# Kernel optimization log

Measured on AMD Instinct MI355X. Metric: run time of the kernel, lower is better.

The kernel has to match this reference:

```python
import jax, jax.numpy as jnp
import numpy as np

HEAD = 12
HEAD_DIM = 64  # dim // head = 768 // 12


def setup_inputs() -> dict:
    key = jax.random.key(0)
    k1, k2, k3 = jax.random.split(key, 3)
    B, N, D = 4, 2048, 768
    scale = 1.0 / np.sqrt(D)
    return {
        "x": jax.random.normal(k1, (B, N, D), dtype=jnp.float32),
        "w_qkv": jax.random.normal(k2, (D, 3 * D), dtype=jnp.float32) * scale,
        "w_proj": jax.random.normal(k3, (D, D), dtype=jnp.float32) * scale,
        "b_proj": jnp.zeros((D,), dtype=jnp.float32),
    }


def reference(x, w_qkv, w_proj, b_proj):
    B, N, D = x.shape
    qkv = x @ w_qkv  # [B, N, 3D]
    q, k, v = jnp.split(qkv, 3, axis=-1)
    # [B, H, N, k]
    def heads(t):
        return t.reshape(B, N, HEAD, HEAD_DIM).transpose(0, 2, 1, 3)
    q, k, v = heads(q), heads(k), heads(v)
    attn = jnp.einsum("bhnd,bhmd->bhnm", q, k) / jnp.sqrt(jnp.float32(HEAD_DIM))
    attn_prob = jax.nn.softmax(attn, axis=-1)  # dropout p=0.0 -> identity
    out = jnp.einsum("bhnm,bhmd->bhnd", attn_prob, v)
    out = out.transpose(0, 2, 1, 3).reshape(B, N, D)
    return out @ w_proj + b_proj
```

## Files before the change

### kernel.cpp

```cpp
#include <hip/hip_runtime.h>

typedef unsigned short u16;
typedef unsigned int u32;
typedef u16 u16x4 __attribute__((ext_vector_type(4)));
typedef u16 u16x8 __attribute__((ext_vector_type(8)));
typedef u32 u32x4 __attribute__((ext_vector_type(4)));
typedef __bf16 bf16x8 __attribute__((ext_vector_type(8)));
typedef float f32x4 __attribute__((ext_vector_type(4)));
typedef float f32x16 __attribute__((ext_vector_type(16)));

#define MFMA16 __builtin_amdgcn_mfma_f32_16x16x32_bf16
#define MFMA32 __builtin_amdgcn_mfma_f32_32x32x16_bf16

__device__ __forceinline__ u16 f2bf(float f) {
  return __builtin_bit_cast(u16, (__bf16)f);
}

__device__ __forceinline__ u32 pk2bf(float a, float b) {
  return (u32)__builtin_bit_cast(u16, (__bf16)a) |
         ((u32)__builtin_bit_cast(u16, (__bf16)b) << 16);
}

__device__ __forceinline__ void gload_lds16(const void* g, void* l) {
  __builtin_amdgcn_global_load_lds(
      (const __attribute__((address_space(1))) u32*)g,
      (__attribute__((address_space(3))) u32*)l, 16, 0, 0);
}

__global__ void cvt_f32_bf16_kernel(const float* __restrict__ in,
                                    u16* __restrict__ out, int n4) {
  int i = blockIdx.x * blockDim.x + threadIdx.x;
  if (i >= n4) return;
  float4 v = reinterpret_cast<const float4*>(in)[i];
  u16x4 o;
  o[0] = f2bf(v.x); o[1] = f2bf(v.y); o[2] = f2bf(v.z); o[3] = f2bf(v.w);
  reinterpret_cast<u16x4*>(out)[i] = o;
}

__global__ void transpose_cvt_kernel(const float* __restrict__ w,
                                     u16* __restrict__ wt, int K, int N) {
  __shared__ float t[32][33];
  int bk = blockIdx.x * 32, bn = blockIdx.y * 32;
  int x = threadIdx.x, y = threadIdx.y;
#pragma unroll
  for (int j = 0; j < 32; j += 8)
    t[y + j][x] = w[(size_t)(bk + y + j) * N + bn + x];
  __syncthreads();
#pragma unroll
  for (int j = 0; j < 32; j += 8)
    wt[(size_t)(bn + y + j) * K + bk + x] = f2bf(t[x][y + j]);
}

#define QSCALE 0.18033688011112042f

template <int NTOT, int EPI>
__global__ __launch_bounds__(256)
void gemm_bf16_kernel(const u16* __restrict__ A, const u16* __restrict__ BT,
                      u16* __restrict__ qo, u16* __restrict__ ko,
                      u16* __restrict__ vt, float* __restrict__ outF,
                      const float* __restrict__ bias) {
  __shared__ u16 sh[16384];
  u16* As = sh;
  u16* Bs = sh + 8192;
  const int tid = threadIdx.x;
  const int l = tid & 63, w = tid >> 6;
  const int lr = l & 15, lg = l >> 4;
  const int mtile = blockIdx.x & 63;
  const int ntile = blockIdx.x >> 6;
  const int mbase = mtile * 128, nbase = ntile * 128;
  const int wr = (w >> 1) * 64, wc = (w & 1) * 64;

  f32x4 acc[4][4] = {};

  for (int k0 = 0; k0 < 768; k0 += 64) {
#pragma unroll
    for (int i = 0; i < 4; ++i) {
      const int c = w * 64 + i * 256 + l;
      const int row = c >> 3, c16 = c & 7;
      const int sc = c16 ^ (row & 7);
      gload_lds16(A + (size_t)(mbase + row) * 768 + k0 + sc * 8,
                  &As[(size_t)(w * 64 + i * 256) * 8]);
      gload_lds16(BT + (size_t)(nbase + row) * 768 + k0 + sc * 8,
                  &Bs[(size_t)(w * 64 + i * 256) * 8]);
    }
    __syncthreads();
#pragma unroll
    for (int ks = 0; ks < 2; ++ks) {
      bf16x8 af[4], bfr[4];
#pragma unroll
      for (int m = 0; m < 4; ++m) {
        const int row = wr + m * 16 + lr;
        const int byte = (row * 128 + ks * 64 + lg * 16) ^ ((row & 7) << 4);
        af[m] = *reinterpret_cast<const bf16x8*>((const char*)As + byte);
      }
#pragma unroll
      for (int n = 0; n < 4; ++n) {
        const int row = wc + n * 16 + lr;
        const int byte = (row * 128 + ks * 64 + lg * 16) ^ ((row & 7) << 4);
        bfr[n] = *reinterpret_cast<const bf16x8*>((const char*)Bs + byte);
      }
#pragma unroll
      for (int m = 0; m < 4; ++m)
#pragma unroll
        for (int n = 0; n < 4; ++n)
          acc[m][n] = MFMA16(af[m], bfr[n], acc[m][n], 0, 0, 0);
    }
    __syncthreads();
  }

  if (EPI == 0 && ntile >= 12) {
    u16* vts = sh;
#pragma unroll
    for (int m = 0; m < 4; ++m)
#pragma unroll
      for (int n = 0; n < 4; ++n)
#pragma unroll
        for (int r = 0; r < 4; ++r) {
          const int col = wc + n * 16 + lr;
          const int row = wr + m * 16 + lg * 4 + r;
          const int byte = col * 256 + ((row * 2) ^ ((col & 7) << 4));
          *reinterpret_cast<u16*>((char*)vts + byte) = f2bf(acc[m][n][r]);
        }
    __syncthreads();
    const int b2 = mbase >> 11, nn0 = mbase & 2047;
#pragma unroll
    for (int i = 0; i < 8; ++i) {
      const int idx = i * 256 + tid;
      const int col = idx >> 4, u = idx & 15;
      u16x8 vv = *reinterpret_cast<u16x8*>(
          (char*)vts + (col * 256 + ((u * 16) ^ ((col & 7) << 4))));
      const int cg = nbase - 1536 + col;
      const int hh = cg >> 6, dd = cg & 63;
      *reinterpret_cast<u16x8*>(
          vt + (((size_t)(b2 * 12 + hh)) * 64 + dd) * 2048 + nn0 + u * 8) = vv;
    }
    return;
  }

#pragma unroll
  for (int m = 0; m < 4; ++m) {
#pragma unroll
    for (int n = 0; n < 4; ++n) {
#pragma unroll
      for (int r = 0; r < 4; ++r) {
        const int row = mbase + wr + m * 16 + lg * 4 + r;
        const int col = nbase + wc + n * 16 + lr;
        float val = acc[m][n][r];
        if (EPI == 0) {
          const int w2 = col / 768;
          const int c2 = col - w2 * 768;
          const int hh = c2 >> 6, dd = c2 & 63;
          const int b2 = row >> 11, nn = row & 2047;
          u16* dst = (w2 == 0) ? qo : ko;
          if (w2 == 0) val *= QSCALE;
          dst[(((size_t)(b2 * 12 + hh)) * 2048 + nn) * 64 + dd] = f2bf(val);
        } else {
          outF[(size_t)row * NTOT + col] = val + bias[col];
        }
      }
    }
  }
}

__global__ __launch_bounds__(256)
void flash_attn32_kernel(const u16* __restrict__ qb, const u16* __restrict__ kb,
                         const u16* __restrict__ vtb, u16* __restrict__ ao) {
  __shared__ u16 sh[16384];
  const int tid = threadIdx.x, w = tid >> 6, l = tid & 63;
  const int q5 = l & 31, hi = l >> 5;
  const int swz = (blockIdx.x & 7) * 96 + (blockIdx.x >> 3);
  const int bh = swz >> 4, qt = swz & 15;
  const int b = bh / 12, h = bh % 12;
  const int qrow0 = qt * 128 + w * 32;
  const u16* Q = qb + ((size_t)bh * 2048 + qrow0) * 64;
  const u16* K = kb + (size_t)bh * 2048 * 64;
  const u16* Vg = vtb + (size_t)bh * 64 * 2048;

  bf16x8 qf[4];
#pragma unroll
  for (int dk = 0; dk < 4; ++dk)
    qf[dk] = *reinterpret_cast<const bf16x8*>(Q + (size_t)q5 * 64 + dk * 16 + hi * 8);

  u16x8 ob1;
#pragma unroll
  for (int i = 0; i < 8; ++i) ob1[i] = 0x3F80;
  const bf16x8 ones = __builtin_bit_cast(bf16x8, ob1);

  f32x16 ot0 = {}, ot1 = {};
  f32x16 osum = {};

  auto stage = [&](u16* base, int kt) {
#pragma unroll
    for (int i = 0; i < 2; ++i) {
      const int c = w * 64 + i * 256 + l;
      const int row = c >> 3, sc = (c & 7) ^ (row & 7);
      gload_lds16(K + (size_t)(kt + row) * 64 + sc * 8,
                  base + (size_t)(w * 64 + i * 256) * 8);
    }
#pragma unroll
    for (int i = 0; i < 2; ++i) {
      const int c = w * 64 + i * 256 + l;
      const int row = c >> 3, sc = (c & 7) ^ (row & 7);
      gload_lds16(Vg + (size_t)row * 2048 + kt + sc * 8,
                  base + 4096 + (size_t)(w * 64 + i * 256) * 8);
    }
  };

  stage(sh, 0);
  int cur = 0;
  const int swq = (q5 & 7) << 4;

  for (int kt = 0; kt < 2048; kt += 64) {
    __syncthreads();
    u16* tb = sh + cur * 8192;
    if (kt + 64 < 2048) stage(sh + (cur ^ 1) * 8192, kt + 64);
    const char* ksb = (const char*)tb;
    const char* vsb = (const char*)(tb + 4096);

    f32x16 st0 = {}, st1 = {};
    __builtin_amdgcn_s_setprio(1);
#pragma unroll
    for (int dk = 0; dk < 4; ++dk) {
      const int off = dk * 32 + hi * 16;
      bf16x8 kf0 = *reinterpret_cast<const bf16x8*>(ksb + ((q5 * 128 + off) ^ swq));
      bf16x8 kf1 = *reinterpret_cast<const bf16x8*>(ksb + (((q5 + 32) * 128 + off) ^ swq));
      st0 = MFMA32(kf0, qf[dk], st0, 0, 0, 0);
      st1 = MFMA32(kf1, qf[dk], st1, 0, 0, 0);
    }
    __builtin_amdgcn_s_setprio(0);

#pragma unroll
    for (int r = 0; r < 16; ++r) st0[r] = __builtin_amdgcn_exp2f(st0[r]);
#pragma unroll
    for (int r = 0; r < 16; ++r) st1[r] = __builtin_amdgcn_exp2f(st1[r]);

    __builtin_amdgcn_s_setprio(1);
#pragma unroll
    for (int kvs = 0; kvs < 4; ++kvs) {
      const f32x16& stx = (kvs < 2) ? st0 : st1;
      const int rb = (kvs & 1) * 8;
      const u32 A0 = pk2bf(stx[rb + 0], stx[rb + 1]);
      const u32 A1 = pk2bf(stx[rb + 2], stx[rb + 3]);
      const u32 A2 = pk2bf(stx[rb + 4], stx[rb + 5]);
      const u32 A3 = pk2bf(stx[rb + 6], stx[rb + 7]);
      const u32 s1 = hi ? A0 : A2, s2 = hi ? A1 : A3;
      const u32 r1 = (u32)__shfl_xor((int)s1, 32);
      const u32 r2 = (u32)__shfl_xor((int)s2, 32);
      u32x4 wv;
      wv[0] = hi ? r1 : A0; wv[1] = hi ? r2 : A1;
      wv[2] = hi ? A2 : r1; wv[3] = hi ? A3 : r2;
      const bf16x8 pf = __builtin_bit_cast(bf16x8, wv);
      const int off = kvs * 32 + hi * 16;
      bf16x8 vf0 = *reinterpret_cast<const bf16x8*>(vsb + ((q5 * 128 + off) ^ swq));
      bf16x8 vf1 = *reinterpret_cast<const bf16x8*>(vsb + (((q5 + 32) * 128 + off) ^ swq));
      ot0 = MFMA32(vf0, pf, ot0, 0, 0, 0);
      ot1 = MFMA32(vf1, pf, ot1, 0, 0, 0);
      osum = MFMA32(ones, pf, osum, 0, 0, 0);
    }
    __builtin_amdgcn_s_setprio(0);
    cur ^= 1;
  }

  u16* ob = sh + w * 2048;
  const float inv = 1.0f / osum[0];
#pragma unroll
  for (int g = 0; g < 4; ++g) {
    u16x4 pk0, pk1;
#pragma unroll
    for (int r = 0; r < 4; ++r) {
      pk0[r] = f2bf(ot0[g * 4 + r] * inv);
      pk1[r] = f2bf(ot1[g * 4 + r] * inv);
    }
    const int d0 = hi * 4 + g * 8;
    *reinterpret_cast<u16x4*>((char*)ob + ((q5 * 128 + d0 * 2) ^ swq)) = pk0;
    *reinterpret_cast<u16x4*>((char*)ob + ((q5 * 128 + (d0 + 32) * 2) ^ swq)) = pk1;
  }
  __syncthreads();
#pragma unroll
  for (int i = 0; i < 4; ++i) {
    const int idx = i * 64 + l;
    const int qr = idx >> 3, cc = idx & 7;
    u16x8 vv = *reinterpret_cast<u16x8*>(
        (char*)ob + ((qr * 128 + cc * 16) ^ ((qr & 7) << 4)));
    *reinterpret_cast<u16x8*>(
        ao + ((size_t)(b * 2048 + qrow0 + qr)) * 768 + h * 64 + cc * 8) = vv;
  }
}

extern "C" void kernel_launch(void* const* d_in, const int* in_sizes, int n_in,
                              void* d_out, int out_size, void* d_ws,
                              size_t ws_size, hipStream_t stream) {
  const float* x = (const float*)d_in[0];
  const float* w_qkv = (const float*)d_in[1];
  const float* w_proj = (const float*)d_in[2];
  const float* b_proj = (const float*)d_in[3];
  float* out = (float*)d_out;

  char* ws = (char*)d_ws;
  size_t off = 0;
  auto alloc = [&](size_t bytes) {
    char* p = ws + off;
    off += (bytes + 255) & ~(size_t)255;
    return p;
  };
  u16* xb = (u16*)alloc(8192ull * 768 * 2);
  u16* wqkvT = (u16*)alloc(2304ull * 768 * 2);
  u16* wprojT = (u16*)alloc(768ull * 768 * 2);
  u16* qbuf = (u16*)alloc(48ull * 2048 * 64 * 2);
  u16* kbuf = (u16*)alloc(48ull * 2048 * 64 * 2);
  u16* vtb = (u16*)alloc(48ull * 64 * 2048 * 2);
  u16* aob = (u16*)alloc(8192ull * 768 * 2);
  (void)ws_size; (void)n_in; (void)in_sizes; (void)out_size;

  cvt_f32_bf16_kernel<<<(8192 * 768 / 4) / 256, 256, 0, stream>>>(
      x, xb, 8192 * 768 / 4);
  transpose_cvt_kernel<<<dim3(768 / 32, 2304 / 32), dim3(32, 8), 0, stream>>>(
      w_qkv, wqkvT, 768, 2304);
  transpose_cvt_kernel<<<dim3(768 / 32, 768 / 32), dim3(32, 8), 0, stream>>>(
      w_proj, wprojT, 768, 768);

  gemm_bf16_kernel<2304, 0><<<64 * 18, 256, 0, stream>>>(
      xb, wqkvT, qbuf, kbuf, vtb, nullptr, nullptr);

  flash_attn32_kernel<<<768, 256, 0, stream>>>(qbuf, kbuf, vtb, aob);

  gemm_bf16_kernel<768, 1><<<64 * 6, 256, 0, stream>>>(
      aob, wprojT, nullptr, nullptr, nullptr, out, b_proj);
}
```

Before: 178.5 us.

## Split attention KV range across wave pairs and reduce partial outputs in LDS

```diff
diff --git a/kernel.cpp b/kernel.cpp
--- a/kernel.cpp
+++ b/kernel.cpp
@@ -19,6 +19,11 @@
 __device__ __forceinline__ u32 pk2bf(float a, float b) {
   return (u32)__builtin_bit_cast(u16, (__bf16)a) |
          ((u32)__builtin_bit_cast(u16, (__bf16)b) << 16);
+}
+
+__device__ __forceinline__ float bfsum2(u32 w) {
+  return __builtin_bit_cast(float, w << 16) +
+         __builtin_bit_cast(float, w & 0xFFFF0000u);
 }
 
 __device__ __forceinline__ void gload_lds16(const void* g, void* l) {
@@ -168,10 +173,12 @@
   __shared__ u16 sh[16384];
   const int tid = threadIdx.x, w = tid >> 6, l = tid & 63;
   const int q5 = l & 31, hi = l >> 5;
-  const int swz = (blockIdx.x & 7) * 96 + (blockIdx.x >> 3);
-  const int bh = swz >> 4, qt = swz & 15;
+  const int qw = w & 1, half = w >> 1;
+  const int swz = (blockIdx.x & 7) * 192 + (blockIdx.x >> 3);
+  const int bh = swz >> 5, qt = swz & 31;
   const int b = bh / 12, h = bh % 12;
-  const int qrow0 = qt * 128 + w * 32;
+  const int qrow0 = qt * 64 + qw * 32;
+  const int kvStart = half << 10;
   const u16* Q = qb + ((size_t)bh * 2048 + qrow0) * 64;
   const u16* K = kb + (size_t)bh * 2048 * 64;
   const u16* Vg = vtb + (size_t)bh * 64 * 2048;
@@ -181,41 +188,33 @@
   for (int dk = 0; dk < 4; ++dk)
     qf[dk] = *reinterpret_cast<const bf16x8*>(Q + (size_t)q5 * 64 + dk * 16 + hi * 8);
 
-  u16x8 ob1;
-#pragma unroll
-  for (int i = 0; i < 8; ++i) ob1[i] = 0x3F80;
-  const bf16x8 ones = __builtin_bit_cast(bf16x8, ob1);
-
   f32x16 ot0 = {}, ot1 = {};
-  f32x16 osum = {};
-
-  auto stage = [&](u16* base, int kt) {
-#pragma unroll
-    for (int i = 0; i < 2; ++i) {
-      const int c = w * 64 + i * 256 + l;
+  float l_ = 0.f;
+
+  u16* Ks = sh + half * 8192;
+  u16* Vs = Ks + 4096;
+  const int swq = (q5 & 7) << 4;
+
+  for (int t = 0; t < 16; ++t) {
+    const int kt = kvStart + t * 64;
+#pragma unroll
+    for (int i = 0; i < 4; ++i) {
+      const int c = qw * 64 + i * 128 + l;
       const int row = c >> 3, sc = (c & 7) ^ (row & 7);
       gload_lds16(K + (size_t)(kt + row) * 64 + sc * 8,
-                  base + (size_t)(w * 64 + i * 256) * 8);
-    }
-#pragma unroll
-    for (int i = 0; i < 2; ++i) {
-      const int c = w * 64 + i * 256 + l;
+                  Ks + (size_t)(qw * 64 + i * 128) * 8);
+    }
+#pragma unroll
+    for (int i = 0; i < 4; ++i) {
+      const int c = qw * 64 + i * 128 + l;
       const int row = c >> 3, sc = (c & 7) ^ (row & 7);
       gload_lds16(Vg + (size_t)row * 2048 + kt + sc * 8,
-                  base + 4096 + (size_t)(w * 64 + i * 256) * 8);
-    }
-  };
-
-  stage(sh, 0);
-  int cur = 0;
-  const int swq = (q5 & 7) << 4;
-
-  for (int kt = 0; kt < 2048; kt += 64) {
-    __syncthreads();
-    u16* tb = sh + cur * 8192;
-    if (kt + 64 < 2048) stage(sh + (cur ^ 1) * 8192, kt + 64);
-    const char* ksb = (const char*)tb;
-    const char* vsb = (const char*)(tb + 4096);
+                  Vs + (size_t)(qw * 64 + i * 128) * 8);
+    }
+    __syncthreads();
+
+    const char* ksb = (const char*)Ks;
+    const char* vsb = (const char*)Vs;
 
     f32x16 st0 = {}, st1 = {};
     __builtin_amdgcn_s_setprio(1);
@@ -234,6 +233,7 @@
 #pragma unroll
     for (int r = 0; r < 16; ++r) st1[r] = __builtin_amdgcn_exp2f(st1[r]);
 
+    float ls = 0.f;
     __builtin_amdgcn_s_setprio(1);
 #pragma unroll
     for (int kvs = 0; kvs < 4; ++kvs) {
@@ -243,6 +243,7 @@
       const u32 A1 = pk2bf(stx[rb + 2], stx[rb + 3]);
       const u32 A2 = pk2bf(stx[rb + 4], stx[rb + 5]);
       const u32 A3 = pk2bf(stx[rb + 6], stx[rb + 7]);
+      ls += (bfsum2(A0) + bfsum2(A1)) + (bfsum2(A2) + bfsum2(A3));
       const u32 s1 = hi ? A0 : A2, s2 = hi ? A1 : A3;
       const u32 r1 = (u32)__shfl_xor((int)s1, 32);
       const u32 r2 = (u32)__shfl_xor((int)s2, 32);
@@ -255,35 +256,58 @@
       bf16x8 vf1 = *reinterpret_cast<const bf16x8*>(vsb + (((q5 + 32) * 128 + off) ^ swq));
       ot0 = MFMA32(vf0, pf, ot0, 0, 0, 0);
       ot1 = MFMA32(vf1, pf, ot1, 0, 0, 0);
-      osum = MFMA32(ones, pf, osum, 0, 0, 0);
     }
     __builtin_amdgcn_s_setprio(0);
-    cur ^= 1;
-  }
-
-  u16* ob = sh + w * 2048;
-  const float inv = 1.0f / osum[0];
-#pragma unroll
-  for (int g = 0; g < 4; ++g) {
-    u16x4 pk0, pk1;
-#pragma unroll
-    for (int r = 0; r < 4; ++r) {
-      pk0[r] = f2bf(ot0[g * 4 + r] * inv);
-      pk1[r] = f2bf(ot1[g * 4 + r] * inv);
-    }
-    const int d0 = hi * 4 + g * 8;
-    *reinterpret_cast<u16x4*>((char*)ob + ((q5 * 128 + d0 * 2) ^ swq)) = pk0;
-    *reinterpret_cast<u16x4*>((char*)ob + ((q5 * 128 + (d0 + 32) * 2) ^ swq)) = pk1;
+    l_ += ls + __shfl_xor(ls, 32);
+    __syncthreads();
+  }
+
+  if (half) {
+    float* baseO = (float*)((char*)sh + (size_t)(2 + qw) * 8192);
+#pragma unroll
+    for (int r = 0; r < 16; ++r) baseO[r * 64 + l] = ot0[r];
+#pragma unroll
+    for (int r = 0; r < 16; ++r) baseO[(16 + r) * 64 + l] = ot1[r];
+    ((float*)((char*)sh + 8192))[qw * 64 + l] = l_;
   }
   __syncthreads();
-#pragma unroll
-  for (int i = 0; i < 4; ++i) {
-    const int idx = i * 64 + l;
+  if (!half) {
+    const float* baseO = (const float*)((char*)sh + (size_t)(2 + qw) * 8192);
+#pragma unroll
+    for (int r = 0; r < 16; ++r) ot0[r] += baseO[r * 64 + l];
+#pragma unroll
+    for (int r = 0; r < 16; ++r) ot1[r] += baseO[(16 + r) * 64 + l];
+    l_ += ((const float*)((char*)sh + 8192))[qw * 64 + l];
+  }
+  __syncthreads();
+
+  if (!half) {
+    u16* ob = sh + w * 2048;
+    const float inv = 1.0f / l_;
+#pragma unroll
+    for (int g = 0; g < 4; ++g) {
+      u16x4 pk0, pk1;
+#pragma unroll
+      for (int r = 0; r < 4; ++r) {
+        pk0[r] = f2bf(ot0[g * 4 + r] * inv);
+        pk1[r] = f2bf(ot1[g * 4 + r] * inv);
+      }
+      const int d0 = hi * 4 + g * 8;
+      *reinterpret_cast<u16x4*>((char*)ob + ((q5 * 128 + d0 * 2) ^ swq)) = pk0;
+      *reinterpret_cast<u16x4*>((char*)ob + ((q5 * 128 + (d0 + 32) * 2) ^ swq)) = pk1;
+    }
+  }
+  __syncthreads();
+#pragma unroll
+  for (int i = 0; i < 2; ++i) {
+    const int idx = i * 256 + tid;
     const int qr = idx >> 3, cc = idx & 7;
+    u16* rb = sh + (qr >> 5) * 2048;
+    const int q5r = qr & 31;
     u16x8 vv = *reinterpret_cast<u16x8*>(
-        (char*)ob + ((qr * 128 + cc * 16) ^ ((qr & 7) << 4)));
+        (char*)rb + ((q5r * 128 + cc * 16) ^ ((q5r & 7) << 4)));
     *reinterpret_cast<u16x8*>(
-        ao + ((size_t)(b * 2048 + qrow0 + qr)) * 768 + h * 64 + cc * 8) = vv;
+        ao + ((size_t)(b * 2048 + qt * 64 + qr)) * 768 + h * 64 + cc * 8) = vv;
   }
 }
 
@@ -322,7 +346,7 @@
   gemm_bf16_kernel<2304, 0><<<64 * 18, 256, 0, stream>>>(
       xb, wqkvT, qbuf, kbuf, vtb, nullptr, nullptr);
 
-  flash_attn32_kernel<<<768, 256, 0, stream>>>(qbuf, kbuf, vtb, aob);
+  flash_attn32_kernel<<<1536, 256, 0, stream>>>(qbuf, kbuf, vtb, aob);
 
   gemm_bf16_kernel<768, 1><<<64 * 6, 256, 0, stream>>>(
       aob, wprojT, nullptr, nullptr, nullptr, out, b_proj);
```

Result: faster. 168.5 us (-5.6%).
